# Performance work log

Hardware: AMD Instinct MI355X
Metric: run time of the kernel (lower is better)

The kernel has to match this reference:

```python
import jax, jax.numpy as jnp
import numpy as np


def conv2d(x, w, stride=1, padding=0, dilation=1):
    return jax.lax.conv_general_dilated(
        x, w, (stride, stride), [(padding, padding), (padding, padding)],
        rhs_dilation=(dilation, dilation),
        dimension_numbers=("NCHW", "OIHW", "NCHW"))


def pixel_shuffle(x, r):
    b, C, h, w = x.shape
    c = C // (r * r)
    x = x.reshape(b, c, r, r, h, w)
    x = x.transpose(0, 1, 4, 2, 5, 3)  # b,c,h,r,w,r
    return x.reshape(b, c, h * r, w * r)


def phitphi(x, PhiW, PhiTW, B):
    N = B * B
    outs = []
    for c in range(3):
        phi = conv2d(x[:, c:c + 1], PhiW[:, c:c + 1], stride=B)  # [b,M,h/B,w/B]
        outs.append(conv2d(phi, PhiTW[c * N:(c + 1) * N]))        # [b,N,h/B,w/B]
    temp = jnp.concatenate(outs, axis=1)  # [b,3N,h/B,w/B]
    return pixel_shuffle(temp, B)


def adconv(data, W, para):
    # Faithful to ADConv: route each output channel to dilation argmax(para[c]),
    # output channels grouped by dilation (stable order within a group), each
    # group scaled by mean(para[group, i]) + 1.
    C, T = para.shape
    indexs = jnp.argmax(para, axis=1)              # softmax preserves argmax
    perm = jnp.argsort(indexs)                     # stable: group channels by dilation
    ys = jnp.stack([conv2d(data, W, padding=i + 1, dilation=i + 1)
                    for i in range(T)], axis=0)    # [T,b,C,H,W]
    mask = jax.nn.one_hot(indexs, T, dtype=para.dtype)  # [C,T]
    cnt = jnp.maximum(mask.sum(0), 1.0)
    mul = (para * mask).sum(0) / cnt + 1.0         # [T]
    d = indexs[perm]                               # dilation per output channel
    sel = ys[d, :, perm]                           # [C,b,H,W]
    sel = sel * mul[d][:, None, None, None]
    return sel.transpose(1, 0, 2, 3)               # [b,C,H,W]


def setup_inputs() -> dict:
    key = jax.random.key(0)
    ks = jax.random.split(key, 32)
    B, M, C, H, W, F = 32, 256, 3, 320, 320, 32
    N = B * B
    bsz = 4
    inp = {
        "xprev": jax.random.normal(ks[0], (bsz, C, H, W), jnp.float32),
        "x": jax.random.normal(ks[1], (bsz, C, H, W), jnp.float32),
        "PhiWeight": jax.random.normal(ks[2], (M, C, B, B), jnp.float32) / B,
        "PhiTWeight": jax.random.normal(ks[3], (3 * N, M, 1, 1), jnp.float32) / B,
        "PhiTb": jax.random.normal(ks[4], (bsz, C, H, W), jnp.float32),
        "lambda_step": jnp.float32(0.5),
        "soft_thr": jnp.float32(0.01),
        "t": jnp.float32(1.0),
        "mergeScale": jnp.float32(1.0),
        "conv_D": jax.random.normal(ks[5], (F, 3, 3, 3), jnp.float32) * 0.08,
        "conv3_G": jax.random.normal(ks[6], (3, F, 3, 3), jnp.float32) * 0.08,
        "c1f_w": jax.random.normal(ks[7], (F, F, 3, 3), jnp.float32) * 0.06,
        "c1f_p": jax.random.normal(ks[8], (F, 1), jnp.float32),
        "c2f_w": jax.random.normal(ks[9], (F, F, 3, 3), jnp.float32) * 0.06,
        "c2f_p": jax.random.normal(ks[10], (F, 3), jnp.float32),
        "c1b_w": jax.random.normal(ks[11], (F, F, 3, 3), jnp.float32) * 0.06,
        "c1b_p": jax.random.normal(ks[12], (F, 1), jnp.float32),
        "c2b_w": jax.random.normal(ks[13], (F, F, 3, 3), jnp.float32) * 0.06,
        "c2b_p": jax.random.normal(ks[14], (F, 3), jnp.float32),
        "c1g_w": jax.random.normal(ks[15], (F, F, 3, 3), jnp.float32) * 0.06,
        "c1g_p": jax.random.normal(ks[16], (F, 1), jnp.float32),
        "c2g_w": jax.random.normal(ks[17], (F, F, 3, 3), jnp.float32) * 0.06,
        "c2g_p": jax.random.normal(ks[18], (F, 3), jnp.float32),
        "BLOCK_SIZE": 32,
    }
    return inp


def reference(xprev, x, PhiWeight, PhiTWeight, PhiTb,
              lambda_step, soft_thr, t, mergeScale,
              conv_D, conv3_G,
              c1f_w, c1f_p, c2f_w, c2f_p,
              c1b_w, c1b_p, c2b_w, c2b_p,
              c1g_w, c1g_p, c2g_w, c2g_p,
              BLOCK_SIZE):
    tplus = (1.0 + jnp.sqrt(1.0 + 4.0 * t * t)) / 2.0
    xi = (t - 1.0) / tplus
    deltax = x - xprev
    zeta = x - lambda_step * phitphi(x, PhiWeight, PhiTWeight, BLOCK_SIZE)
    zeta = zeta - lambda_step * xi * phitphi(deltax, PhiWeight, PhiTWeight, BLOCK_SIZE)
    zeta = zeta + xi * deltax + lambda_step * PhiTb
    x_input = zeta

    x_D = conv2d(x_input, conv_D, padding=1)
    h = jax.nn.relu(adconv(x_D, c1f_w, c1f_p))
    x_forward = adconv(h, c2f_w, c2f_p)
    # soft threshold
    xs = jnp.sign(x_forward) * jax.nn.relu(jnp.abs(x_forward) - soft_thr)
    h = jax.nn.relu(adconv(xs, c1f_w, c1f_p))  # source reuses conv1_forward here
    x_backward = adconv(h, c2b_w, c2b_p)
    h = adconv(jax.nn.relu(x_backward), c1g_w, c1g_p)
    h = adconv(jax.nn.relu(h), c2g_w, c2g_p)
    x_G = conv2d(h, conv3_G, padding=1)
    x_pred = x_input + x_G * mergeScale

    h = jax.nn.relu(adconv(x_forward, c1b_w, c1b_p))
    x_D_est = adconv(h, c2b_w, c2b_p)
    symloss = x_D_est - x_D
    return (x_pred, symloss)
```

## Files before the change

kernel.cpp:

```cpp
#include <hip/hip_runtime.h>
#include <math.h>

#define HW 320
#define IMGSZ (HW*HW)
#define NB 4

typedef __bf16 bf16x8 __attribute__((ext_vector_type(8)));
typedef float  f32x4  __attribute__((ext_vector_type(4)));

__device__ __forceinline__ float4 ld4(const float* p){ return *reinterpret_cast<const float4*>(p); }

__device__ __forceinline__ unsigned short f2b(float f){
  unsigned u = __float_as_uint(f);
  unsigned r = (u + 0x7fffu + ((u>>16)&1u)) >> 16;
  return (unsigned short)r;
}

__global__ void meta_kernel(const float* p0,const float* p1,const float* p2,
                            const float* p3,const float* p4,const float* p5,
                            int* msrc,int* md,float* mscale,int* pres){
  if (threadIdx.x != 0) return;
  int set = blockIdx.x;
  const float* ps[6] = {p0,p1,p2,p3,p4,p5};
  const int Ts[6] = {1,3,1,3,1,3};
  const float* para = ps[set];
  int T = Ts[set];
  int idx[32]; float mx[32];
  for (int c=0;c<32;c++){
    int best=0; float bv=para[c*T];
    for (int t=1;t<T;t++){ float v=para[c*T+t]; if (v>bv){bv=v;best=t;} }
    idx[c]=best; mx[c]=bv;
  }
  float sum[3]={0.f,0.f,0.f}; int cnt[3]={0,0,0};
  for (int c=0;c<32;c++){ sum[idx[c]] += mx[c]; cnt[idx[c]]++; }
  float mul[3];
  for (int t=0;t<3;t++) mul[t] = sum[t]/fmaxf((float)cnt[t],1.f)+1.f;
  int off[3]; off[0]=0; off[1]=cnt[0]; off[2]=cnt[0]+cnt[1];
  int perm[32];
  for (int c=0;c<32;c++) perm[off[idx[c]]++] = c;
  int pb = 0;
  for (int k=0;k<32;k++){
    int s = perm[k];
    msrc[set*32+k]=s; md[set*32+k]=idx[s]+1; mscale[set*32+k]=mul[idx[s]];
    pb |= 1 << (idx[s]+1);
  }
  pres[set] = pb;
}

__global__ void ew_u(const float* __restrict__ x, const float* __restrict__ xprev,
                     const float* __restrict__ t_p, float* __restrict__ u, int n4){
  int i = blockIdx.x*blockDim.x + threadIdx.x;
  if (i >= n4) return;
  float t = *t_p;
  float tplus = (1.f + sqrtf(1.f + 4.f*t*t)) * 0.5f;
  float xi = (t - 1.f)/tplus;
  float4 xv = ld4(x + 4*i); float4 pv = ld4(xprev + 4*i);
  float4 r;
  r.x = xv.x + xi*(xv.x-pv.x);
  r.y = xv.y + xi*(xv.y-pv.y);
  r.z = xv.z + xi*(xv.z-pv.z);
  r.w = xv.w + xi*(xv.w-pv.w);
  *reinterpret_cast<float4*>(u + 4*i) = r;
}


__global__ void pack_phib(const float* __restrict__ PhiW, uint4* __restrict__ PhiB){
  int idx = blockIdx.x*256 + threadIdx.x;
  int lane = idx & 63;
  int t2 = idx >> 6;
  int nf = t2 & 3, ks = (t2>>2)&31, cm = t2>>7;
  int m = (cm&3)*64 + nf*16 + (lane&15);
  int c = cm>>2;
  int kbase = ks*32 + (lane>>4)*8;
  const float* src = PhiW + ((size_t)m*3 + c)*1024 + kbase;
  float4 v0 = ld4(src), v1 = ld4(src+4);
  float vals[8] = {v0.x,v0.y,v0.z,v0.w,v1.x,v1.y,v1.z,v1.w};
  uint4 hi, lo; unsigned* hw = (unsigned*)&hi; unsigned* lw = (unsigned*)&lo;
  #pragma unroll
  for (int p=0;p<4;p++){
    unsigned h0 = f2b(vals[2*p]), h1 = f2b(vals[2*p+1]);
    float r0 = vals[2*p]   - __uint_as_float(h0<<16);
    float r1 = vals[2*p+1] - __uint_as_float(h1<<16);
    hw[p] = h0 | (h1<<16);
    lw[p] = (unsigned)f2b(r0) | ((unsigned)f2b(r1)<<16);
  }
  PhiB[(size_t)t2*128 + lane] = hi;
  PhiB[(size_t)t2*128 + 64 + lane] = lo;
}

__global__ void pack_phitb(const float* __restrict__ PhiTW, uint4* __restrict__ PhiTB){
  int idx = blockIdx.x*256 + threadIdx.x;
  int lane = idx & 63;
  int t2 = idx >> 6;
  int nf = t2 & 3, ks = (t2>>2)&7, cn = t2>>5;
  int n = (cn&15)*64 + nf*16 + (lane&15);
  int c = cn>>4;
  int kbase = ks*32 + (lane>>4)*8;
  const float* src = PhiTW + ((size_t)c*1024 + n)*256 + kbase;
  float4 v0 = ld4(src), v1 = ld4(src+4);
  float vals[8] = {v0.x,v0.y,v0.z,v0.w,v1.x,v1.y,v1.z,v1.w};
  uint4 hi, lo; unsigned* hw = (unsigned*)&hi; unsigned* lw = (unsigned*)&lo;
  #pragma unroll
  for (int p=0;p<4;p++){
    unsigned h0 = f2b(vals[2*p]), h1 = f2b(vals[2*p+1]);
    float r0 = vals[2*p]   - __uint_as_float(h0<<16);
    float r1 = vals[2*p+1] - __uint_as_float(h1<<16);
    hw[p] = h0 | (h1<<16);
    lw[p] = (unsigned)f2b(r0) | ((unsigned)f2b(r1)<<16);
  }
  PhiTB[(size_t)t2*128 + lane] = hi;
  PhiTB[(size_t)t2*128 + 64 + lane] = lo;
}

__global__ __launch_bounds__(256)
void phi_gemm(const float* __restrict__ u, const uint4* __restrict__ PhiB,
              uint4* __restrict__ PhA){
  __shared__ uint4 As[2][2048];
  const int rt = blockIdx.x, mt = blockIdx.y, c = blockIdx.z;
  const int tid = threadIdx.x, lane = tid & 63, w = tid >> 6;

  for (int idx = tid; idx < 4096; idx += 256){
    int m = idx >> 8;
    int f4 = idx & 255;
    int k = f4*4;
    int r = rt*16 + m;
    int b = r/100, blk = r - b*100;
    int bh = blk/10, bw = blk - bh*10;
    int ip = k >> 5, jp = k & 31;
    float4 v = ld4(u + ((size_t)((b*3+c)*HW + bh*32+ip))*HW + bw*32 + jp);
    float vv[4] = {v.x,v.y,v.z,v.w};
    unsigned hh[4], ll[4];
    #pragma unroll
    for (int e=0;e<4;e++){
      hh[e] = f2b(vv[e]);
      ll[e] = f2b(vv[e] - __uint_as_float(hh[e]<<16));
    }
    int kb = k >> 3, off = (k & 7) ? 1 : 0;
    ((uint2*)&As[0][kb*16+m])[off] = make_uint2(hh[0]|(hh[1]<<16), hh[2]|(hh[3]<<16));
    ((uint2*)&As[1][kb*16+m])[off] = make_uint2(ll[0]|(ll[1]<<16), ll[2]|(ll[3]<<16));
  }
  __syncthreads();

  f32x4 acc[4] = {};
  const uint4* bbase = PhiB + (size_t)(c*4+mt)*32*512;
  for (int ksl = 0; ksl < 8; ++ksl){
    int ks = w*8 + ksl;
    bf16x8 ah = __builtin_bit_cast(bf16x8, As[0][ks*64 + lane]);
    bf16x8 al = __builtin_bit_cast(bf16x8, As[1][ks*64 + lane]);
    #pragma unroll
    for (int nf=0; nf<4; ++nf){
      const uint4* bp = bbase + ((size_t)ks*4 + nf)*128;
      bf16x8 bh = __builtin_bit_cast(bf16x8, bp[lane]);
      bf16x8 bl = __builtin_bit_cast(bf16x8, bp[64 + lane]);
      acc[nf] = __builtin_amdgcn_mfma_f32_16x16x32_bf16(ah, bh, acc[nf], 0,0,0);
      acc[nf] = __builtin_amdgcn_mfma_f32_16x16x32_bf16(ah, bl, acc[nf], 0,0,0);
      acc[nf] = __builtin_amdgcn_mfma_f32_16x16x32_bf16(al, bh, acc[nf], 0,0,0);
    }
  }

  __syncthreads();
  float* rf = (float*)As;
  #pragma unroll
  for (int nf=0; nf<4; ++nf)
    ((float4*)rf)[(w*64+lane)*4 + nf] = *(float4*)&acc[nf];
  __syncthreads();

  int o = tid*4;
  int i = o >> 6, j = o & 63;
  int nf = j >> 4, q = i >> 2, reg = i & 3;
  unsigned hh[4], ll[4];
  #pragma unroll
  for (int e=0;e<4;e++){
    int ls = q*16 + (j&15) + e;
    float v = rf[(0*64+ls)*16 + nf*4+reg] + rf[(1*64+ls)*16 + nf*4+reg]
            + rf[(2*64+ls)*16 + nf*4+reg] + rf[(3*64+ls)*16 + nf*4+reg];
    hh[e] = f2b(v);
    ll[e] = f2b(v - __uint_as_float(hh[e]<<16));
  }
  int kb = mt*8 + (j>>3);
  int off = (j & 7) ? 1 : 0;
  ((uint2*)&PhA[((size_t)(0*3+c)*25 + rt)*512 + kb*16 + i])[off] =
      make_uint2(hh[0]|(hh[1]<<16), hh[2]|(hh[3]<<16));
  ((uint2*)&PhA[((size_t)(1*3+c)*25 + rt)*512 + kb*16 + i])[off] =
      make_uint2(ll[0]|(ll[1]<<16), ll[2]|(ll[3]<<16));
}

__global__ __launch_bounds__(256)
void phit_gemm(const uint4* __restrict__ PhA, const uint4* __restrict__ PhiTB,
               const float* __restrict__ u, const float* __restrict__ PhiTb,
               const float* __restrict__ lam_p, float* __restrict__ x_input){
  const int rt = blockIdx.x, nt4 = blockIdx.y, c = blockIdx.z;
  const int tid = threadIdx.x, lane = tid & 63, w = tid >> 6;
  f32x4 acc[4] = {};
  const uint4* ah_base = PhA + ((size_t)(0*3+c)*25 + rt)*512;
  const uint4* al_base = PhA + ((size_t)(1*3+c)*25 + rt)*512;
  const uint4* bbase = PhiTB + (size_t)(c*16 + nt4*4 + w)*8*512;
  #pragma unroll
  for (int ks=0; ks<8; ++ks){
    bf16x8 ah = __builtin_bit_cast(bf16x8, ah_base[ks*64 + lane]);
    bf16x8 al = __builtin_bit_cast(bf16x8, al_base[ks*64 + lane]);
    #pragma unroll
    for (int nf=0; nf<4; ++nf){
      const uint4* bp = bbase + ((size_t)ks*4 + nf)*128;
      bf16x8 bh = __builtin_bit_cast(bf16x8, bp[lane]);
      bf16x8 bl = __builtin_bit_cast(bf16x8, bp[64 + lane]);
      acc[nf] = __builtin_amdgcn_mfma_f32_16x16x32_bf16(ah, bh, acc[nf], 0,0,0);
      acc[nf] = __builtin_amdgcn_mfma_f32_16x16x32_bf16(ah, bl, acc[nf], 0,0,0);
      acc[nf] = __builtin_amdgcn_mfma_f32_16x16x32_bf16(al, bh, acc[nf], 0,0,0);
    }
  }
  float lam = *lam_p;
  int q = lane >> 4, jl = lane & 15;
  #pragma unroll
  for (int nf=0; nf<4; ++nf){
    int n = nt4*256 + w*64 + nf*16 + jl;
    int ip = n >> 5, jp = n & 31;
    #pragma unroll
    for (int reg=0; reg<4; ++reg){
      int r = rt*16 + q*4 + reg;
      int b = r/100, blk = r - b*100;
      int bh_ = blk/10, bw_ = blk - bh_*10;
      size_t g = ((size_t)((b*3+c)*HW + bh_*32+ip))*HW + bw_*32 + jp;
      x_input[g] = u[g] - lam*acc[nf][reg] + lam*PhiTb[g];
    }
  }
}

__global__ __launch_bounds__(256)
void conv_direct_blocked(const float* __restrict__ in, const float* __restrict__ wts,
                         uint4* __restrict__ dst){
  const int tile = blockIdx.x, g = blockIdx.y, b = blockIdx.z;
  const int x0 = (tile % 20)*16, y0 = (tile / 20)*16;
  const int tid = threadIdx.x;
  __shared__ float ism[3*18*20];
  __shared__ float wsm[8*27];
  for (int i = tid; i < 3*18*18; i += 256){
    int ic = i / 324; int rr = i - ic*324; int r = rr/18, c = rr - r*18;
    int gy = y0 - 1 + r, gx = x0 - 1 + c;
    float v = 0.f;
    if (gy>=0 && gy<HW && gx>=0 && gx<HW)
      v = in[(size_t)(b*3+ic)*IMGSZ + (size_t)gy*HW + gx];
    ism[(ic*18+r)*20 + c] = v;
  }
  if (tid < 216) wsm[tid] = wts[(size_t)(g*8 + tid/27)*27 + (tid%27)];
  __syncthreads();

  const int px = tid & 15, py = tid >> 4;
  float acc[8] = {};
  #pragma unroll
  for (int ic=0; ic<3; ++ic)
    #pragma unroll
    for (int ky=0; ky<3; ++ky)
      #pragma unroll
      for (int kx=0; kx<3; ++kx){
        float v = ism[(ic*18+py+ky)*20 + px+kx];
        #pragma unroll
        for (int o=0;o<8;o++)
          acc[o] += wsm[o*27 + ic*9 + ky*3 + kx] * v;
      }
  uint4 ov; unsigned* ow = (unsigned*)&ov;
  #pragma unroll
  for (int p=0;p<4;p++)
    ow[p] = (unsigned)f2b(acc[2*p]) | ((unsigned)f2b(acc[2*p+1])<<16);
  dst[(((size_t)(b*4+g)*HW + (y0+py))*HW + x0+px)] = ov;
}

__global__ void pack_w(const float* w0,const float* w1,const float* w2,
                       const float* w3,const float* w4,const float* w5,
                       const float* w6,
                       const int* msrc,const int* md,const float* mscale,
                       uint4* __restrict__ wp){
  const float* wsel[7] = {w0,w1,w2,w3,w4,w5,w6};
  const int set_of[13]  = {0,1,1,1,2,3,3,3,4,5,5,5,6};
  const int cls_of[13]  = {1,1,2,3,1,1,2,3,1,1,2,3,1};
  int slot = blockIdx.x;
  int set = set_of[slot], cls = cls_of[slot];
  const float* W = wsel[set];
  unsigned short* out = (unsigned short*)(wp + (size_t)slot*1152);
  for (int v = threadIdx.x; v < 9216; v += 256){
    int j = v & 7;
    int lane = (v >> 3) & 63;
    int rest = v >> 9;
    int t = rest % 9, h = rest / 9;
    int ocl = lane & 15, q = lane >> 4;
    int oc = h*16 + ocl;
    int ic = q*8 + j;
    float val = 0.f;
    if (set == 6){
      if (oc < 3) val = W[(size_t)oc*(32*9) + ic*9 + t];
    } else {
      if (md[set*32+oc] == cls){
        int src = msrc[set*32+oc];
        val = W[(size_t)src*(32*9) + ic*9 + t] * mscale[set*32+oc];
      }
    }
    out[v] = f2b(val);
  }
}

template<int H,int NPASS,int NH,int ROWS,int ITRANS,int EPI>
__device__ __forceinline__ void conv_body(char* smem,
    const uint4* __restrict__ inb, const uint4* __restrict__ wp,
    void* __restrict__ outp, const int* __restrict__ pres_p, int set,
    const float* __restrict__ thr_p, const float* __restrict__ epi_ptr,
    const float* __restrict__ ms_p, int tx, int ty, int b){
  constexpr int TW = 32 + 2*H, TH = ROWS + 2*H, TP = TW*TH;
  constexpr int RPW = ROWS/4;
  constexpr int MT  = ROWS/2;
  constexpr int PW  = ROWS*8;

  const int x0 = tx*32, y0 = ty*ROWS;
  const int tid = threadIdx.x;
  const int lane = tid & 63, w = tid >> 6;
  const int m = lane & 15, q = lane >> 4;

  float thr = (ITRANS==2) ? *thr_p : 0.f;
  uint4* sm16 = (uint4*)smem;
  constexpr int TOT = 4*TP;
  constexpr int NSTG = (TOT + 255)/256;
  for (int base = 0; base < NSTG; base += 4){
    uint4 v[4];
    #pragma unroll
    for (int uu=0; uu<4; ++uu){
      v[uu] = make_uint4(0,0,0,0);
      if (base+uu < NSTG){
        int i = tid + (base+uu)*256;
        if (i < TOT){
          int g = i / TP; int rr = i - g*TP; int r = rr / TW; int c = rr - r*TW;
          int gy = y0 - H + r, gx = x0 - H + c;
          if (gy>=0 && gy<HW && gx>=0 && gx<HW)
            v[uu] = inb[(((size_t)(b*4+g)*HW + gy)*HW + gx)];
        }
      }
    }
    #pragma unroll
    for (int uu=0; uu<4; ++uu){
      if (base+uu < NSTG){
        int i = tid + (base+uu)*256;
        if (i < TOT){
          uint4 vv = v[uu];
          if (ITRANS==1){
            unsigned* pw = (unsigned*)&vv;
            #pragma unroll
            for (int z=0;z<4;z++){
              unsigned lo = pw[z] & 0xffffu, hi = pw[z] >> 16;
              if (lo & 0x8000u) lo = 0;
              if (hi & 0x8000u) hi = 0;
              pw[z] = lo | (hi<<16);
            }
          } else if (ITRANS==2){
            unsigned* pw = (unsigned*)&vv;
            #pragma unroll
            for (int z=0;z<4;z++){
              unsigned lo = pw[z] & 0xffffu, hi = pw[z] >> 16;
              float f0 = __uint_as_float(lo<<16), f1 = __uint_as_float(hi<<16);
              float a0 = fabsf(f0)-thr, a1 = fabsf(f1)-thr;
              f0 = (a0>0.f)? copysignf(a0,f0) : 0.f;
              f1 = (a1>0.f)? copysignf(a1,f1) : 0.f;
              pw[z] = (unsigned)f2b(f0) | ((unsigned)f2b(f1)<<16);
            }
          }
          sm16[i] = vv;
        }
      }
    }
  }
  __syncthreads();

  f32x4 acc[MT][NH] = {};
  int pres = (NPASS==3) ? pres_p[set] : 2;
  for (int d = 1; d <= NPASS; ++d){
    if (NPASS==3 && !((pres>>d)&1)) continue;
    const uint4* wbase = wp + (size_t)(d-1)*1152;
    bf16x8 bcur[NH];
    #pragma unroll
    for (int h=0; h<NH; ++h)
      bcur[h] = __builtin_bit_cast(bf16x8, wbase[(h*9 + 0)*64 + lane]);
    for (int t = 0; t < 9; ++t){
      bf16x8 bnxt[NH];
      if (t < 8){
        #pragma unroll
        for (int h=0; h<NH; ++h)
          bnxt[h] = __builtin_bit_cast(bf16x8, wbase[(h*9 + t+1)*64 + lane]);
      }
      int dy = (t/3 - 1)*d, dx = (t%3 - 1)*d;
      const uint4* sp = sm16 + q*TP + (H+dy)*TW + H + dx;
      #pragma unroll
      for (int mt=0; mt<MT; ++mt){
        int r = mt >> 1, xh = mt & 1;
        bf16x8 a = __builtin_bit_cast(bf16x8, sp[(w*RPW + r)*TW + xh*16 + m]);
        #pragma unroll
        for (int h=0; h<NH; ++h)
          acc[mt][h] = __builtin_amdgcn_mfma_f32_16x16x32_bf16(a, bcur[h], acc[mt][h], 0,0,0);
      }
      if (t < 8){
        #pragma unroll
        for (int h=0; h<NH; ++h) bcur[h] = bnxt[h];
      }
    }
  }

  if (EPI == 2){
    float ms = *ms_p;
    #pragma unroll
    for (int mt=0; mt<MT; ++mt){
      int r = mt >> 1, xh = mt & 1;
      int y = y0 + w*RPW + r;
      int x = x0 + xh*16 + q*4;
      #pragma unroll
      for (int h=0; h<NH; ++h){
        int oc = h*16 + m;
        if (oc < 3){
          size_t off = (((size_t)(b*3+oc)*HW + y)*HW + x);
          float4 e = ld4(epi_ptr + off);
          float4 o;
          o.x = e.x + ms*acc[mt][h][0];
          o.y = e.y + ms*acc[mt][h][1];
          o.z = e.z + ms*acc[mt][h][2];
          o.w = e.w + ms*acc[mt][h][3];
          *reinterpret_cast<float4*>((float*)outp + off) = o;
        }
      }
    }
  } else if (EPI == 3){
    __syncthreads();
    float* swf = (float*)smem + (size_t)w*(PW*33);
    #pragma unroll
    for (int mt=0; mt<MT; ++mt){
      int r = mt >> 1, xh = mt & 1;
      #pragma unroll
      for (int h=0; h<NH; ++h){
        int oc = h*16 + m;
        #pragma unroll
        for (int reg=0; reg<4; ++reg){
          int P = r*32 + xh*16 + q*4 + reg;
          swf[P*33 + oc] = acc[mt][h][reg];
        }
      }
    }
    int row = lane >> 5, col = lane & 31;
    int y = y0 + w*RPW + row, x = x0 + col;
    const uint4* xb = (const uint4*)epi_ptr;
    float xd[32];
    #pragma unroll
    for (int g2=0; g2<4; ++g2){
      uint4 vv = xb[(((size_t)(b*4+g2)*HW + y)*HW + x)];
      const unsigned short* sp16 = (const unsigned short*)&vv;
      #pragma unroll
      for (int ci=0; ci<8; ++ci)
        xd[g2*8+ci] = __uint_as_float(((unsigned)sp16[ci])<<16);
    }
    float* out1f = (float*)outp;
    #pragma unroll
    for (int oc=0; oc<32; ++oc){
      float v = swf[lane*33 + oc] - xd[oc];
      out1f[(((size_t)(b*32+oc)*HW + y)*HW + x)] = v;
    }
  } else {
    __syncthreads();
    short* sw = (short*)smem + (size_t)w*PW*40;
    #pragma unroll
    for (int mt=0; mt<MT; ++mt){
      int r = mt >> 1, xh = mt & 1;
      #pragma unroll
      for (int h=0; h<NH; ++h){
        int oc = h*16 + m;
        #pragma unroll
        for (int reg=0; reg<4; ++reg){
          float v = acc[mt][h][reg];
          if (EPI==1) v = fmaxf(v, 0.f);
          int P = r*32 + xh*16 + q*4 + reg;
          sw[P*40 + oc] = (short)f2b(v);
        }
      }
    }
    #pragma unroll
    for (int i=0; i<PW/16; ++i){
      int id = i*64 + lane;
      int g2 = id / PW, P = id % PW;
      uint4 val = *reinterpret_cast<uint4*>(&sw[P*40 + g2*8]);
      int y2 = y0 + w*RPW + (P>>5), x2 = x0 + (P&31);
      ((uint4*)outp)[(((size_t)(b*4+g2)*HW + y2)*HW + x2)] = val;
    }
  }
}

template<int EPI,int ROWS> struct epi_lds {
  static constexpr int SE = (EPI<=1) ? ROWS*8*40*2*4 : (EPI==3 ? ROWS*8*33*4*4 : 0);
};

template<int H,int NPASS,int NH,int ITRANS,int EPI,int ROWS>
__global__ __launch_bounds__(256, 2)
void mfma_conv_s(const uint4* __restrict__ inb, const uint4* __restrict__ wp,
                 void* __restrict__ outp,
                 const int* __restrict__ pres_p, int set,
                 const float* __restrict__ thr_p,
                 const float* __restrict__ epi_ptr,
                 const float* __restrict__ ms_p){
  constexpr int TP = (32+2*H)*(ROWS+2*H);
  constexpr int S1 = 4*TP*16;
  constexpr int S2 = epi_lds<EPI,ROWS>::SE;
  constexpr int SB = S1 > S2 ? S1 : S2;
  __shared__ __align__(16) char smem[SB];
  conv_body<H,NPASS,NH,ROWS,ITRANS,EPI>(smem, inb, wp, outp, pres_p, set,
                                        thr_p, epi_ptr, ms_p,
                                        blockIdx.x, blockIdx.y, blockIdx.z);
}

template<int H,int NPASS,int NH,int ROWS,int IT0,int EP0,int IT1,int EP1>
__global__ __launch_bounds__(256, 2)
void mfma_conv_d(const uint4* __restrict__ in0, const uint4* __restrict__ in1,
                 const uint4* __restrict__ wp0, const uint4* __restrict__ wp1,
                 void* __restrict__ o0, void* __restrict__ o1,
                 const int* __restrict__ pres_p, int set,
                 const float* __restrict__ thr_p,
                 const float* __restrict__ e0, const float* __restrict__ e1,
                 const float* __restrict__ ms_p){
  constexpr int TP = (32+2*H)*(ROWS+2*H);
  constexpr int S1 = 4*TP*16;
  constexpr int SE0 = epi_lds<EP0,ROWS>::SE;
  constexpr int SE1 = epi_lds<EP1,ROWS>::SE;
  constexpr int S2 = SE0 > SE1 ? SE0 : SE1;
  constexpr int SB = S1 > S2 ? S1 : S2;
  __shared__ __align__(16) char smem[SB];
  int b = blockIdx.z & 3, job = blockIdx.z >> 2;
  if (job == 0)
    conv_body<H,NPASS,NH,ROWS,IT0,EP0>(smem, in0, wp0, o0, pres_p, set,
                                       thr_p, e0, ms_p, blockIdx.x, blockIdx.y, b);
  else
    conv_body<H,NPASS,NH,ROWS,IT1,EP1>(smem, in1, wp1, o1, pres_p, set,
                                       thr_p, e1, ms_p, blockIdx.x, blockIdx.y, b);
}

extern "C" void kernel_launch(void* const* d_in, const int* in_sizes, int n_in,
                              void* d_out, int out_size, void* d_ws, size_t ws_size,
                              hipStream_t stream) {
  const float* xprev = (const float*)d_in[0];
  const float* x     = (const float*)d_in[1];
  const float* PhiW  = (const float*)d_in[2];
  const float* PhiTW = (const float*)d_in[3];
  const float* PhiTb = (const float*)d_in[4];
  const float* lam   = (const float*)d_in[5];
  const float* sthr  = (const float*)d_in[6];
  const float* t_p   = (const float*)d_in[7];
  const float* mrg   = (const float*)d_in[8];
  const float* convD = (const float*)d_in[9];
  const float* conv3G= (const float*)d_in[10];
  const float* c1f_w=(const float*)d_in[11]; const float* c1f_p=(const float*)d_in[12];
  const float* c2f_w=(const float*)d_in[13]; const float* c2f_p=(const float*)d_in[14];
  const float* c1b_w=(const float*)d_in[15]; const float* c1b_p=(const float*)d_in[16];
  const float* c2b_w=(const float*)d_in[17]; const float* c2b_p=(const float*)d_in[18];
  const float* c1g_w=(const float*)d_in[19]; const float* c1g_p=(const float*)d_in[20];
  const float* c2g_w=(const float*)d_in[21]; const float* c2g_p=(const float*)d_in[22];

  char* ws = (char*)d_ws;
  const size_t BL = (size_t)NB*4*IMGSZ*16;
  uint4* xDb = (uint4*)(ws + 0*BL);
  uint4* Bb  = (uint4*)(ws + 1*BL);
  uint4* Cb  = (uint4*)(ws + 2*BL);
  uint4* Db  = (uint4*)(ws + 3*BL);
  uint4* Eb  = (uint4*)(ws + 4*BL);
  float* xDf = (float*)(ws + 5*BL);
  float* x_input = (float*)(ws + 5*BL + 52428800);
  float* u       = (float*)(ws + 5*BL + 52428800 + 4915200);
  char*  phir    = ws + 5*BL + 52428800 + 2*4915200;
  uint4* PhiB    = (uint4*)phir;
  uint4* PhA     = (uint4*)(phir + 3145728);
  uint4* PhiTB   = (uint4*)xDf;
  uint4* Wp      = (uint4*)(ws + 5*BL + 52428800 + 3*4915200);
  char*  mbase   = ws + 5*BL + 52428800 + 3*4915200 + 13*18432;
  int*   msrc    = (int*)(mbase);
  int*   md      = (int*)(mbase + 768);
  float* mscale  = (float*)(mbase + 2*768);
  int*   pres    = (int*)(mbase + 3*768);

  float* out0 = (float*)d_out;
  float* out1 = out0 + (size_t)NB*3*IMGSZ;

  meta_kernel<<<6, 64, 0, stream>>>(c1f_p,c2f_p,c1b_p,c2b_p,c1g_p,c2g_p,
                                    msrc, md, mscale, pres);
  pack_w<<<13, 256, 0, stream>>>(c1f_w,c2f_w,c1b_w,c2b_w,c1g_w,c2g_w,conv3G,
                                 msrc, md, mscale, Wp);
  pack_phib<<<384, 256, 0, stream>>>(PhiW, PhiB);
  pack_phitb<<<384, 256, 0, stream>>>(PhiTW, PhiTB);

  ew_u<<<1200, 256, 0, stream>>>(x, xprev, t_p, u, 307200);
  phi_gemm<<<dim3(25,4,3), 256, 0, stream>>>(u, PhiB, PhA);
  phit_gemm<<<dim3(25,4,3), 256, 0, stream>>>(PhA, PhiTB, u, PhiTb, lam, x_input);

  conv_direct_blocked<<<dim3(400,4,NB), 256, 0, stream>>>(x_input, convD, xDb);

  dim3 mg(10,40,NB);
  dim3 mg2(10,40,NB*2);
  uint4* W_c1f = Wp + 0*1152;
  uint4* W_c2f = Wp + 1*1152;
  uint4* W_c1b = Wp + 4*1152;
  uint4* W_c2b = Wp + 5*1152;
  uint4* W_c1g = Wp + 8*1152;
  uint4* W_c2g = Wp + 9*1152;
  uint4* W_g3  = Wp + 12*1152;

  mfma_conv_s<1,1,2,0,1,8><<<mg,256,0,stream>>>(xDb, W_c1f, Bb, nullptr,0, nullptr,nullptr,nullptr);
  mfma_conv_s<3,3,2,0,0,8><<<mg,256,0,stream>>>(Bb, W_c2f, Cb, pres,1, nullptr,nullptr,nullptr);
  mfma_conv_d<1,1,2,8, 2,1, 0,1><<<mg2,256,0,stream>>>(Cb, Cb, W_c1f, W_c1b, Db, Bb,
                                                       nullptr,0, sthr, nullptr,nullptr, nullptr);
  mfma_conv_d<3,3,2,8, 0,0, 0,3><<<mg2,256,0,stream>>>(Db, Bb, W_c2b, W_c2b, Eb, out1,
                                                       pres,3, nullptr, nullptr, (const float*)xDb, nullptr);
  mfma_conv_s<1,1,2,1,0,8><<<mg,256,0,stream>>>(Eb, W_c1g, Db, nullptr,0, nullptr,nullptr,nullptr);
  mfma_conv_s<3,3,2,1,0,8><<<mg,256,0,stream>>>(Db, W_c2g, Eb, pres,5, nullptr,nullptr,nullptr);
  mfma_conv_s<1,1,1,0,2,8><<<mg,256,0,stream>>>(Eb, W_g3, out0, nullptr,0, nullptr, x_input, mrg);
}
```

Before: 409.7 us.

## Fold metadata into pack_w, pad LDS epilogue stride, move ReLU into epilogues

Merges the adconv metadata computation into the weight-packing kernel, which removes one launch and the global metadata buffers. It also fully unrolls the halo tile staging into a single load/store pass and changes the epilogue LDS row stride from 40 to 44 shorts to cut bank conflicts, reading rows back with 8-byte loads. ReLU on the backward path moves from the input transform of the next conv into the producing conv's epilogue via template flags. The larger unrolled staging raises register pressure, and the padded stride grows the shared-memory footprint.

New measurement: 392.3 us. -4.2%, faster.

```diff
diff --git a/kernel.cpp b/kernel.cpp
--- a/kernel.cpp
+++ b/kernel.cpp
@@ -14,37 +14,6 @@
   unsigned u = __float_as_uint(f);
   unsigned r = (u + 0x7fffu + ((u>>16)&1u)) >> 16;
   return (unsigned short)r;
-}
-
-__global__ void meta_kernel(const float* p0,const float* p1,const float* p2,
-                            const float* p3,const float* p4,const float* p5,
-                            int* msrc,int* md,float* mscale,int* pres){
-  if (threadIdx.x != 0) return;
-  int set = blockIdx.x;
-  const float* ps[6] = {p0,p1,p2,p3,p4,p5};
-  const int Ts[6] = {1,3,1,3,1,3};
-  const float* para = ps[set];
-  int T = Ts[set];
-  int idx[32]; float mx[32];
-  for (int c=0;c<32;c++){
-    int best=0; float bv=para[c*T];
-    for (int t=1;t<T;t++){ float v=para[c*T+t]; if (v>bv){bv=v;best=t;} }
-    idx[c]=best; mx[c]=bv;
-  }
-  float sum[3]={0.f,0.f,0.f}; int cnt[3]={0,0,0};
-  for (int c=0;c<32;c++){ sum[idx[c]] += mx[c]; cnt[idx[c]]++; }
-  float mul[3];
-  for (int t=0;t<3;t++) mul[t] = sum[t]/fmaxf((float)cnt[t],1.f)+1.f;
-  int off[3]; off[0]=0; off[1]=cnt[0]; off[2]=cnt[0]+cnt[1];
-  int perm[32];
-  for (int c=0;c<32;c++) perm[off[idx[c]]++] = c;
-  int pb = 0;
-  for (int k=0;k<32;k++){
-    int s = perm[k];
-    msrc[set*32+k]=s; md[set*32+k]=idx[s]+1; mscale[set*32+k]=mul[idx[s]];
-    pb |= 1 << (idx[s]+1);
-  }
-  pres[set] = pb;
 }
 
 __global__ void ew_u(const float* __restrict__ x, const float* __restrict__ xprev,
@@ -268,13 +237,47 @@
 __global__ void pack_w(const float* w0,const float* w1,const float* w2,
                        const float* w3,const float* w4,const float* w5,
                        const float* w6,
-                       const int* msrc,const int* md,const float* mscale,
-                       uint4* __restrict__ wp){
+                       const float* p0,const float* p1,const float* p2,
+                       const float* p3,const float* p4,const float* p5,
+                       int* __restrict__ pres, uint4* __restrict__ wp){
   const float* wsel[7] = {w0,w1,w2,w3,w4,w5,w6};
+  const float* psel[6] = {p0,p1,p2,p3,p4,p5};
   const int set_of[13]  = {0,1,1,1,2,3,3,3,4,5,5,5,6};
   const int cls_of[13]  = {1,1,2,3,1,1,2,3,1,1,2,3,1};
+  const int Ts[6] = {1,3,1,3,1,3};
   int slot = blockIdx.x;
   int set = set_of[slot], cls = cls_of[slot];
+
+  __shared__ int   s_src[32];
+  __shared__ int   s_d[32];
+  __shared__ float s_scale[32];
+
+  if (set < 6 && threadIdx.x == 0){
+    const float* para = psel[set];
+    int T = Ts[set];
+    int idx[32]; float mx[32];
+    for (int c=0;c<32;c++){
+      int best=0; float bv=para[c*T];
+      for (int t=1;t<T;t++){ float v=para[c*T+t]; if (v>bv){bv=v;best=t;} }
+      idx[c]=best; mx[c]=bv;
+    }
+    float sum[3]={0.f,0.f,0.f}; int cnt[3]={0,0,0};
+    for (int c=0;c<32;c++){ sum[idx[c]] += mx[c]; cnt[idx[c]]++; }
+    float mul[3];
+    for (int t=0;t<3;t++) mul[t] = sum[t]/fmaxf((float)cnt[t],1.f)+1.f;
+    int off[3]; off[0]=0; off[1]=cnt[0]; off[2]=cnt[0]+cnt[1];
+    int perm[32];
+    for (int c=0;c<32;c++) perm[off[idx[c]]++] = c;
+    int pb = 0;
+    for (int k=0;k<32;k++){
+      int s = perm[k];
+      s_src[k]=s; s_d[k]=idx[s]+1; s_scale[k]=mul[idx[s]];
+      pb |= 1 << (idx[s]+1);
+    }
+    if (cls == 1) pres[set] = pb;
+  }
+  __syncthreads();
+
   const float* W = wsel[set];
   unsigned short* out = (unsigned short*)(wp + (size_t)slot*1152);
   for (int v = threadIdx.x; v < 9216; v += 256){
@@ -289,9 +292,9 @@
     if (set == 6){
       if (oc < 3) val = W[(size_t)oc*(32*9) + ic*9 + t];
     } else {
-      if (md[set*32+oc] == cls){
-        int src = msrc[set*32+oc];
-        val = W[(size_t)src*(32*9) + ic*9 + t] * mscale[set*32+oc];
+      if (s_d[oc] == cls){
+        int src = s_src[oc];
+        val = W[(size_t)src*(32*9) + ic*9 + t] * s_scale[oc];
       }
     }
     out[v] = f2b(val);
@@ -318,50 +321,46 @@
   uint4* sm16 = (uint4*)smem;
   constexpr int TOT = 4*TP;
   constexpr int NSTG = (TOT + 255)/256;
-  for (int base = 0; base < NSTG; base += 4){
-    uint4 v[4];
-    #pragma unroll
-    for (int uu=0; uu<4; ++uu){
+  {
+    uint4 v[NSTG];
+    #pragma unroll
+    for (int uu=0; uu<NSTG; ++uu){
       v[uu] = make_uint4(0,0,0,0);
-      if (base+uu < NSTG){
-        int i = tid + (base+uu)*256;
-        if (i < TOT){
-          int g = i / TP; int rr = i - g*TP; int r = rr / TW; int c = rr - r*TW;
-          int gy = y0 - H + r, gx = x0 - H + c;
-          if (gy>=0 && gy<HW && gx>=0 && gx<HW)
-            v[uu] = inb[(((size_t)(b*4+g)*HW + gy)*HW + gx)];
+      int i = tid + uu*256;
+      if (i < TOT){
+        int g = i / TP; int rr = i - g*TP; int r = rr / TW; int c = rr - r*TW;
+        int gy = y0 - H + r, gx = x0 - H + c;
+        if (gy>=0 && gy<HW && gx>=0 && gx<HW)
+          v[uu] = inb[(((size_t)(b*4+g)*HW + gy)*HW + gx)];
+      }
+    }
+    #pragma unroll
+    for (int uu=0; uu<NSTG; ++uu){
+      int i = tid + uu*256;
+      if (i < TOT){
+        uint4 vv = v[uu];
+        if (ITRANS==1){
+          unsigned* pw = (unsigned*)&vv;
+          #pragma unroll
+          for (int z=0;z<4;z++){
+            unsigned lo = pw[z] & 0xffffu, hi = pw[z] >> 16;
+            if (lo & 0x8000u) lo = 0;
+            if (hi & 0x8000u) hi = 0;
+            pw[z] = lo | (hi<<16);
+          }
+        } else if (ITRANS==2){
+          unsigned* pw = (unsigned*)&vv;
+          #pragma unroll
+          for (int z=0;z<4;z++){
+            unsigned lo = pw[z] & 0xffffu, hi = pw[z] >> 16;
+            float f0 = __uint_as_float(lo<<16), f1 = __uint_as_float(hi<<16);
+            float a0 = fabsf(f0)-thr, a1 = fabsf(f1)-thr;
+            f0 = (a0>0.f)? copysignf(a0,f0) : 0.f;
+            f1 = (a1>0.f)? copysignf(a1,f1) : 0.f;
+            pw[z] = (unsigned)f2b(f0) | ((unsigned)f2b(f1)<<16);
+          }
         }
-      }
-    }
-    #pragma unroll
-    for (int uu=0; uu<4; ++uu){
-      if (base+uu < NSTG){
-        int i = tid + (base+uu)*256;
-        if (i < TOT){
-          uint4 vv = v[uu];
-          if (ITRANS==1){
-            unsigned* pw = (unsigned*)&vv;
-            #pragma unroll
-            for (int z=0;z<4;z++){
-              unsigned lo = pw[z] & 0xffffu, hi = pw[z] >> 16;
-              if (lo & 0x8000u) lo = 0;
-              if (hi & 0x8000u) hi = 0;
-              pw[z] = lo | (hi<<16);
-            }
-          } else if (ITRANS==2){
-            unsigned* pw = (unsigned*)&vv;
-            #pragma unroll
-            for (int z=0;z<4;z++){
-              unsigned lo = pw[z] & 0xffffu, hi = pw[z] >> 16;
-              float f0 = __uint_as_float(lo<<16), f1 = __uint_as_float(hi<<16);
-              float a0 = fabsf(f0)-thr, a1 = fabsf(f1)-thr;
-              f0 = (a0>0.f)? copysignf(a0,f0) : 0.f;
-              f1 = (a1>0.f)? copysignf(a1,f1) : 0.f;
-              pw[z] = (unsigned)f2b(f0) | ((unsigned)f2b(f1)<<16);
-            }
-          }
-          sm16[i] = vv;
-        }
+        sm16[i] = vv;
       }
     }
   }
@@ -458,7 +457,7 @@
     }
   } else {
     __syncthreads();
-    short* sw = (short*)smem + (size_t)w*PW*40;
+    short* sw = (short*)smem + (size_t)w*PW*44;
     #pragma unroll
     for (int mt=0; mt<MT; ++mt){
       int r = mt >> 1, xh = mt & 1;
@@ -470,15 +469,18 @@
           float v = acc[mt][h][reg];
           if (EPI==1) v = fmaxf(v, 0.f);
           int P = r*32 + xh*16 + q*4 + reg;
-          sw[P*40 + oc] = (short)f2b(v);
+          sw[P*44 + oc] = (short)f2b(v);
         }
       }
     }
+    const uint2* sw2 = (const uint2*)sw;
     #pragma unroll
     for (int i=0; i<PW/16; ++i){
       int id = i*64 + lane;
       int g2 = id / PW, P = id % PW;
-      uint4 val = *reinterpret_cast<uint4*>(&sw[P*40 + g2*8]);
+      uint2 v0 = sw2[P*11 + g2*2];
+      uint2 v1 = sw2[P*11 + g2*2 + 1];
+      uint4 val = make_uint4(v0.x, v0.y, v1.x, v1.y);
       int y2 = y0 + w*RPW + (P>>5), x2 = x0 + (P&31);
       ((uint4*)outp)[(((size_t)(b*4+g2)*HW + y2)*HW + x2)] = val;
     }
@@ -486,7 +488,7 @@
 }
 
 template<int EPI,int ROWS> struct epi_lds {
-  static constexpr int SE = (EPI<=1) ? ROWS*8*40*2*4 : (EPI==3 ? ROWS*8*33*4*4 : 0);
+  static constexpr int SE = (EPI<=1) ? ROWS*8*44*2*4 : (EPI==3 ? ROWS*8*33*4*4 : 0);
 };
 
 template<int H,int NPASS,int NH,int ITRANS,int EPI,int ROWS>
@@ -569,22 +571,18 @@
   uint4* PhiTB   = (uint4*)xDf;
   uint4* Wp      = (uint4*)(ws + 5*BL + 52428800 + 3*4915200);
   char*  mbase   = ws + 5*BL + 52428800 + 3*4915200 + 13*18432;
-  int*   msrc    = (int*)(mbase);
-  int*   md      = (int*)(mbase + 768);
-  float* mscale  = (float*)(mbase + 2*768);
-  int*   pres    = (int*)(mbase + 3*768);
+  int*   pres    = (int*)(mbase);
 
   float* out0 = (float*)d_out;
   float* out1 = out0 + (size_t)NB*3*IMGSZ;
 
-  meta_kernel<<<6, 64, 0, stream>>>(c1f_p,c2f_p,c1b_p,c2b_p,c1g_p,c2g_p,
-                                    msrc, md, mscale, pres);
-  pack_w<<<13, 256, 0, stream>>>(c1f_w,c2f_w,c1b_w,c2b_w,c1g_w,c2g_w,conv3G,
-                                 msrc, md, mscale, Wp);
+  ew_u<<<1200, 256, 0, stream>>>(x, xprev, t_p, u, 307200);
   pack_phib<<<384, 256, 0, stream>>>(PhiW, PhiB);
   pack_phitb<<<384, 256, 0, stream>>>(PhiTW, PhiTB);
-
-  ew_u<<<1200, 256, 0, stream>>>(x, xprev, t_p, u, 307200);
+  pack_w<<<13, 256, 0, stream>>>(c1f_w,c2f_w,c1b_w,c2b_w,c1g_w,c2g_w,conv3G,
+                                 c1f_p,c2f_p,c1b_p,c2b_p,c1g_p,c2g_p,
+                                 pres, Wp);
+
   phi_gemm<<<dim3(25,4,3), 256, 0, stream>>>(u, PhiB, PhA);
   phit_gemm<<<dim3(25,4,3), 256, 0, stream>>>(PhA, PhiTB, u, PhiTb, lam, x_input);
 
@@ -604,9 +602,9 @@
   mfma_conv_s<3,3,2,0,0,8><<<mg,256,0,stream>>>(Bb, W_c2f, Cb, pres,1, nullptr,nullptr,nullptr);
   mfma_conv_d<1,1,2,8, 2,1, 0,1><<<mg2,256,0,stream>>>(Cb, Cb, W_c1f, W_c1b, Db, Bb,
                                                        nullptr,0, sthr, nullptr,nullptr, nullptr);
-  mfma_conv_d<3,3,2,8, 0,0, 0,3><<<mg2,256,0,stream>>>(Db, Bb, W_c2b, W_c2b, Eb, out1,
+  mfma_conv_d<3,3,2,8, 0,1, 0,3><<<mg2,256,0,stream>>>(Db, Bb, W_c2b, W_c2b, Eb, out1,
                                                        pres,3, nullptr, nullptr, (const float*)xDb, nullptr);
-  mfma_conv_s<1,1,2,1,0,8><<<mg,256,0,stream>>>(Eb, W_c1g, Db, nullptr,0, nullptr,nullptr,nullptr);
-  mfma_conv_s<3,3,2,1,0,8><<<mg,256,0,stream>>>(Db, W_c2g, Eb, pres,5, nullptr,nullptr,nullptr);
+  mfma_conv_s<1,1,2,0,1,8><<<mg,256,0,stream>>>(Eb, W_c1g, Db, nullptr,0, nullptr,nullptr,nullptr);
+  mfma_conv_s<3,3,2,0,0,8><<<mg,256,0,stream>>>(Db, W_c2g, Eb, pres,5, nullptr,nullptr,nullptr);
   mfma_conv_s<1,1,1,0,2,8><<<mg,256,0,stream>>>(Eb, W_g3, out0, nullptr,0, nullptr, x_input, mrg);
 }
```
